# Performance work log

Hardware: AMD Instinct MI355X
Metric: run time of the kernel (lower is better)

The kernel has to match this reference:

```python
import jax, jax.numpy as jnp
import numpy as np

B, S, D_MODEL, H, OUT = 32, 64, 256, 256, 10
N_POS = 64  # n_max_seq + 1


def _coordinate_map():
    i = jnp.arange(N_POS, dtype=jnp.float32)
    r = jnp.sqrt(jnp.float32(N_POS))
    c0 = (i / r - 2.0) / 2.0
    c1 = (jnp.mod(i, r) - 2.0) / 2.0
    coord = jnp.stack([c0, c1], axis=-1)            # [N_POS, 2]
    return jnp.broadcast_to(coord[None], (B, N_POS, 2))


def setup_inputs() -> dict:
    key = jax.random.key(0)
    ks = jax.random.split(key, 13)
    d_in = (D_MODEL + 2) * 3
    w = lambda k, i, o: jax.random.normal(k, (i, o), jnp.float32) * 0.02
    b = lambda k, o: jax.random.normal(k, (o,), jnp.float32) * 0.02
    return {
        'sentences': jax.random.normal(ks[0], (B, S, D_MODEL), jnp.float32),
        'coord': _coordinate_map(),
        'g_w1': w(ks[1], d_in, H), 'g_b1': b(ks[2], H),
        'g_w2': w(ks[3], H, H),    'g_b2': b(ks[4], H),
        'g_w3': w(ks[5], H, H),    'g_b3': b(ks[6], H),
        'f_w1': w(ks[7], H, H),    'f_b1': b(ks[8], H),
        'f_w2': w(ks[9], H, H),    'f_b2': b(ks[10], H),
        'f_w3': w(ks[11], H, OUT), 'f_b3': b(ks[12], OUT),
    }


def reference(sentences, coord, g_w1, g_b1, g_w2, g_b2, g_w3, g_b3,
              f_w1, f_b1, f_w2, f_b2, f_w3, f_b3):
    b, s, d = sentences.shape
    x = jnp.concatenate([sentences, coord[:b, :s, :]], axis=-1)   # [B,S,D+2]
    oi = jnp.broadcast_to(x[:, None, :, :], (b, s, s, d + 2))     # object_i[b,i,j]=x[b,j]
    oj = jnp.broadcast_to(x[:, :, None, :], (b, s, s, d + 2))     # object_j[b,i,j]=x[b,i]
    pairs = jnp.concatenate([oi, oj, oi * oj], axis=-1)           # [B,S,S,3*(D+2)]
    h = jax.nn.relu(jnp.einsum('bijk,kh->bijh', pairs, g_w1) + g_b1)
    h = jax.nn.relu(h @ g_w2 + g_b2)
    h = jax.nn.relu(h @ g_w3 + g_b3)
    rel = h.reshape(b, s * s, -1).sum(axis=1)                     # [B,H]
    y = jax.nn.relu(rel @ f_w1 + f_b1)
    y = jax.nn.relu(y @ f_w2 + f_b2)                              # Dropout: eval mode (identity)
    return y @ f_w3 + f_b3                                        # [B,OUT]
```

## Files before the change

kernel.cpp:

```cpp
#include <hip/hip_runtime.h>
#include <hip/hip_bf16.h>


typedef __attribute__((ext_vector_type(4))) float f32x4;
typedef __attribute__((ext_vector_type(8))) short frag8;

__device__ __forceinline__ float bf2f(short s) {
  return __uint_as_float(((unsigned)(unsigned short)s) << 16);
}
__device__ __forceinline__ short f2bf(float f) {
  unsigned u = __float_as_uint(f);
  return (short)((u + 0x7fffu + ((u >> 16) & 1u)) >> 16);
}

#define KX 288

__global__ __launch_bounds__(256)
void prep(const float* __restrict__ sent, const float* __restrict__ coord,
          const float* __restrict__ g_w1, const float* __restrict__ g_w2,
          const float* __restrict__ g_w3,
          short* __restrict__ xb, short* __restrict__ Wab, short* __restrict__ Wc,
          short* __restrict__ W2t, short* __restrict__ W3t, float* __restrict__ rel) {
  __shared__ short tile[64 * 66];
  const int blk = blockIdx.x, t = threadIdx.x;

  if (blk < 288) {
    long idx0 = ((long)blk * 256 + t) * 8;
#pragma unroll
    for (int e = 0; e < 8; e++) {
      long idx = idx0 + e;
      int row = (int)(idx / KX), k = (int)(idx - (long)row * KX);
      float v = 0.f;
      if (k < 256)      v = sent[(size_t)row * 256 + k];
      else if (k < 258) v = coord[row * 2 + (k - 256)];
      xb[idx] = f2bf(v);
    }
    return;
  }

  const int nc = t & 63, r4 = t >> 6;
  if (blk < 328) {
    int tt = blk - 288, kt = tt >> 3, nt = tt & 7;
    int k0 = kt * 64, n0 = nt * 64;
    for (int p = 0; p < 16; p++) {
      int kl = p * 4 + r4, k = k0 + kl, n = n0 + nc;
      float v = 0.f;
      if (k < 258) {
        int row = (n < 256) ? k : 258 + k;
        int col = (n < 256) ? n : n - 256;
        v = g_w1[(size_t)row * 256 + col];
      }
      tile[kl * 66 + nc] = f2bf(v);
    }
    __syncthreads();
    for (int p = 0; p < 16; p++) {
      int nl = p * 4 + r4;
      if (k0 + nc < KX) Wab[(size_t)(n0 + nl) * KX + k0 + nc] = tile[nc * 66 + nl];
    }
    return;
  }
  if (blk < 348) {
    int tt = blk - 328, kt = tt >> 2, nt = tt & 3;
    int k0 = kt * 64, n0 = nt * 64;
    for (int p = 0; p < 16; p++) {
      int kl = p * 4 + r4, k = k0 + kl;
      float v = (k < 258) ? g_w1[(size_t)(516 + k) * 256 + n0 + nc] : 0.f;
      tile[kl * 66 + nc] = f2bf(v);
    }
    __syncthreads();
    for (int p = 0; p < 16; p++) {
      int nl = p * 4 + r4;
      if (k0 + nc < KX) Wc[(size_t)(n0 + nl) * KX + k0 + nc] = tile[nc * 66 + nl];
    }
    return;
  }
  if (blk < 380) {
    int tt = blk - 348;
    const float* W = (tt < 16) ? g_w2 : g_w3;
    short* Wt = (tt < 16) ? W2t : W3t;
    tt &= 15;
    int k0 = (tt >> 2) * 64, n0 = (tt & 3) * 64;
    for (int p = 0; p < 16; p++) {
      int kl = p * 4 + r4;
      tile[kl * 66 + nc] = f2bf(W[(size_t)(k0 + kl) * 256 + n0 + nc]);
    }
    __syncthreads();
    for (int p = 0; p < 16; p++) {
      int nl = p * 4 + r4;
      Wt[(size_t)(n0 + nl) * 256 + k0 + nc] = tile[nc * 66 + nl];
    }
    return;
  }
  {
    int bb = blk - 380;
    ((f32x4*)rel)[bb * 256 + t] = (f32x4){0.f, 0.f, 0.f, 0.f};
  }
}


__global__ __launch_bounds__(64)
void uv_gemm(const short* __restrict__ xb, const short* __restrict__ Wab,
             const float* __restrict__ g_b1, float* __restrict__ uv) {
  const int m0 = blockIdx.x * 64;
  const int n0 = blockIdx.y * 64;
  const int lane = threadIdx.x;
  const int q = lane >> 4, l16 = lane & 15;

  f32x4 acc[4][4];
#pragma unroll
  for (int mt = 0; mt < 4; mt++)
#pragma unroll
    for (int nt = 0; nt < 4; nt++) acc[mt][nt] = (f32x4){0.f, 0.f, 0.f, 0.f};

  for (int k0 = 0; k0 < KX; k0 += 32) {
    frag8 a[4], bb[4];
#pragma unroll
    for (int mt = 0; mt < 4; mt++)
      a[mt] = *(const frag8*)(xb + (size_t)(m0 + mt * 16 + l16) * KX + k0 + q * 8);
#pragma unroll
    for (int nt = 0; nt < 4; nt++)
      bb[nt] = *(const frag8*)(Wab + (size_t)(n0 + nt * 16 + l16) * KX + k0 + q * 8);
#pragma unroll
    for (int mt = 0; mt < 4; mt++)
#pragma unroll
      for (int nt = 0; nt < 4; nt++)
        acc[mt][nt] = __builtin_amdgcn_mfma_f32_16x16x32_bf16(a[mt], bb[nt], acc[mt][nt], 0, 0, 0);
  }
#pragma unroll
  for (int nt = 0; nt < 4; nt++) {
    int col = n0 + nt * 16 + l16;
    float bias = (col >= 256) ? g_b1[col - 256] : 0.f;
#pragma unroll
    for (int mt = 0; mt < 4; mt++) {
      int m = m0 + mt * 16 + q * 4;
#pragma unroll
      for (int r = 0; r < 4; r++)
        uv[(size_t)(m + r) * 512 + col] = acc[mt][nt][r] + bias;
    }
  }
}


#define AS 296
#define LDS_SHORTS (64 * AS)

__global__ __launch_bounds__(256, 3)
void relnet_main(const short* __restrict__ xb, const short* __restrict__ Wc,
                 const short* __restrict__ W2t, const short* __restrict__ W3t,
                 const float* __restrict__ uv, const float* __restrict__ g_b2,
                 const float* __restrict__ g_b3, float* __restrict__ rel) {
  __shared__ short lds[LDS_SHORTS];

  const int tid = threadIdx.x;
  const int bi = blockIdx.x;
  const int b = bi >> 6, i = bi & 63;
  const int lane = tid & 63, wave = tid >> 6;
  const int q = lane >> 4, l16 = lane & 15;
  const int n0 = wave * 64;
  const int rowbase = b * 64;
  const short* xi = xb + (size_t)(rowbase + i) * KX;

  f32x4 acc[4][4];
#pragma unroll
  for (int mt = 0; mt < 4; mt++)
#pragma unroll
    for (int nt = 0; nt < 4; nt++) acc[mt][nt] = (f32x4){0.f, 0.f, 0.f, 0.f};

#pragma unroll
  for (int it = 0; it < 9; it++) {
    int idx = tid + it * 256;
    int j = idx / 36, k8 = (idx - j * 36) * 8;
    frag8 aj = *(const frag8*)(xb + (size_t)(rowbase + j) * KX + k8);
    frag8 ai = *(const frag8*)(xi + k8);
    frag8 r;
#pragma unroll
    for (int t = 0; t < 8; t++) r[t] = f2bf(bf2f(aj[t]) * bf2f(ai[t]));
    *(frag8*)(&lds[j * AS + k8]) = r;
  }
  __syncthreads();

  {
    frag8 a0[4], b0[4], a1[4], b1[4];
#pragma unroll
    for (int mt = 0; mt < 4; mt++)
      a0[mt] = *(const frag8*)(&lds[(mt * 16 + l16) * AS + q * 8]);
#pragma unroll
    for (int nt = 0; nt < 4; nt++)
      b0[nt] = *(const frag8*)(Wc + (size_t)(n0 + nt * 16 + l16) * KX + q * 8);
#pragma unroll
    for (int ks = 0; ks < 9; ks++) {
      if (ks < 8) {
        int k1 = (ks + 1) * 32;
#pragma unroll
        for (int mt = 0; mt < 4; mt++)
          a1[mt] = *(const frag8*)(&lds[(mt * 16 + l16) * AS + k1 + q * 8]);
#pragma unroll
        for (int nt = 0; nt < 4; nt++)
          b1[nt] = *(const frag8*)(Wc + (size_t)(n0 + nt * 16 + l16) * KX + k1 + q * 8);
      }
#pragma unroll
      for (int mt = 0; mt < 4; mt++)
#pragma unroll
        for (int nt = 0; nt < 4; nt++)
          acc[mt][nt] = __builtin_amdgcn_mfma_f32_16x16x32_bf16(a0[mt], b0[nt], acc[mt][nt], 0, 0, 0);
#pragma unroll
      for (int mt = 0; mt < 4; mt++) a0[mt] = a1[mt];
#pragma unroll
      for (int nt = 0; nt < 4; nt++) b0[nt] = b1[nt];
    }
  }
  __syncthreads();

  {
    const float* ub = uv + (size_t)rowbase * 512;
    const float* vp = uv + (size_t)(rowbase + i) * 512 + 256;
#pragma unroll
    for (int nt = 0; nt < 4; nt++) {
      int col = n0 + nt * 16 + l16;
      float vv = vp[col];
#pragma unroll
      for (int mt = 0; mt < 4; mt++) {
        int jb = mt * 16 + q * 4;
#pragma unroll
        for (int r = 0; r < 4; r++) {
          float val = acc[mt][nt][r] + ub[(size_t)(jb + r) * 512 + col] + vv;
          lds[(jb + r) * AS + col] = f2bf(fmaxf(val, 0.f));
        }
        acc[mt][nt] = (f32x4){0.f, 0.f, 0.f, 0.f};
      }
    }
  }
  __syncthreads();

  {
    frag8 a0[4], b0[4], a1[4], b1[4];
#pragma unroll
    for (int mt = 0; mt < 4; mt++)
      a0[mt] = *(const frag8*)(&lds[(mt * 16 + l16) * AS + q * 8]);
#pragma unroll
    for (int nt = 0; nt < 4; nt++)
      b0[nt] = *(const frag8*)(W2t + (size_t)(n0 + nt * 16 + l16) * 256 + q * 8);
#pragma unroll
    for (int ks = 0; ks < 8; ks++) {
      if (ks < 7) {
        int k1 = (ks + 1) * 32;
#pragma unroll
        for (int mt = 0; mt < 4; mt++)
          a1[mt] = *(const frag8*)(&lds[(mt * 16 + l16) * AS + k1 + q * 8]);
#pragma unroll
        for (int nt = 0; nt < 4; nt++)
          b1[nt] = *(const frag8*)(W2t + (size_t)(n0 + nt * 16 + l16) * 256 + k1 + q * 8);
      }
#pragma unroll
      for (int mt = 0; mt < 4; mt++)
#pragma unroll
        for (int nt = 0; nt < 4; nt++)
          acc[mt][nt] = __builtin_amdgcn_mfma_f32_16x16x32_bf16(a0[mt], b0[nt], acc[mt][nt], 0, 0, 0);
#pragma unroll
      for (int mt = 0; mt < 4; mt++) a0[mt] = a1[mt];
#pragma unroll
      for (int nt = 0; nt < 4; nt++) b0[nt] = b1[nt];
    }
  }
  __syncthreads();
#pragma unroll
  for (int nt = 0; nt < 4; nt++) {
    int col = n0 + nt * 16 + l16;
    float b2 = g_b2[col];
#pragma unroll
    for (int mt = 0; mt < 4; mt++) {
      int jb = mt * 16 + q * 4;
#pragma unroll
      for (int r = 0; r < 4; r++)
        lds[(jb + r) * AS + col] = f2bf(fmaxf(acc[mt][nt][r] + b2, 0.f));
      acc[mt][nt] = (f32x4){0.f, 0.f, 0.f, 0.f};
    }
  }
  __syncthreads();

  {
    frag8 a0[4], b0[4], a1[4], b1[4];
#pragma unroll
    for (int mt = 0; mt < 4; mt++)
      a0[mt] = *(const frag8*)(&lds[(mt * 16 + l16) * AS + q * 8]);
#pragma unroll
    for (int nt = 0; nt < 4; nt++)
      b0[nt] = *(const frag8*)(W3t + (size_t)(n0 + nt * 16 + l16) * 256 + q * 8);
#pragma unroll
    for (int ks = 0; ks < 8; ks++) {
      if (ks < 7) {
        int k1 = (ks + 1) * 32;
#pragma unroll
        for (int mt = 0; mt < 4; mt++)
          a1[mt] = *(const frag8*)(&lds[(mt * 16 + l16) * AS + k1 + q * 8]);
#pragma unroll
        for (int nt = 0; nt < 4; nt++)
          b1[nt] = *(const frag8*)(W3t + (size_t)(n0 + nt * 16 + l16) * 256 + k1 + q * 8);
      }
#pragma unroll
      for (int mt = 0; mt < 4; mt++)
#pragma unroll
        for (int nt = 0; nt < 4; nt++)
          acc[mt][nt] = __builtin_amdgcn_mfma_f32_16x16x32_bf16(a0[mt], b0[nt], acc[mt][nt], 0, 0, 0);
#pragma unroll
      for (int mt = 0; mt < 4; mt++) a0[mt] = a1[mt];
#pragma unroll
      for (int nt = 0; nt < 4; nt++) b0[nt] = b1[nt];
    }
  }
#pragma unroll
  for (int nt = 0; nt < 4; nt++) {
    int col = n0 + nt * 16 + l16;
    float b3 = g_b3[col];
    float s = 0.f;
#pragma unroll
    for (int mt = 0; mt < 4; mt++)
#pragma unroll
      for (int r = 0; r < 4; r++)
        s += fmaxf(acc[mt][nt][r] + b3, 0.f);
    s += __shfl_xor(s, 16, 64);
    s += __shfl_xor(s, 32, 64);
    if (q == 0) atomicAdd(&rel[b * 256 + col], s);
  }
}

__global__ __launch_bounds__(256)
void fnet(const float* __restrict__ rel, const float* __restrict__ f_w1,
          const float* __restrict__ f_b1, const float* __restrict__ f_w2,
          const float* __restrict__ f_b2, const float* __restrict__ f_w3,
          const float* __restrict__ f_b3, float* __restrict__ out) {
  int b = blockIdx.x, t = threadIdx.x;
  __shared__ float y0[256], y1[256], y2[256];
  y0[t] = rel[b * 256 + t];
  __syncthreads();
  float s = f_b1[t];
#pragma unroll 8
  for (int k = 0; k < 256; k++) s += y0[k] * f_w1[k * 256 + t];
  y1[t] = fmaxf(s, 0.f);
  __syncthreads();
  s = f_b2[t];
#pragma unroll 8
  for (int k = 0; k < 256; k++) s += y1[k] * f_w2[k * 256 + t];
  y2[t] = fmaxf(s, 0.f);
  __syncthreads();
  if (t < 10) {
    float s2 = f_b3[t];
#pragma unroll 8
    for (int k = 0; k < 256; k++) s2 += y2[k] * f_w3[k * 10 + t];
    out[b * 10 + t] = s2;
  }
}

extern "C" void kernel_launch(void* const* d_in, const int* in_sizes, int n_in,
                              void* d_out, int out_size, void* d_ws, size_t ws_size,
                              hipStream_t stream) {
  const float* sent  = (const float*)d_in[0];
  const float* coord = (const float*)d_in[1];
  const float* g_w1  = (const float*)d_in[2];
  const float* g_b1  = (const float*)d_in[3];
  const float* g_w2  = (const float*)d_in[4];
  const float* g_b2  = (const float*)d_in[5];
  const float* g_w3  = (const float*)d_in[6];
  const float* g_b3  = (const float*)d_in[7];
  const float* f_w1  = (const float*)d_in[8];
  const float* f_b1  = (const float*)d_in[9];
  const float* f_w2  = (const float*)d_in[10];
  const float* f_b2  = (const float*)d_in[11];
  const float* f_w3  = (const float*)d_in[12];
  const float* f_b3  = (const float*)d_in[13];
  float* out = (float*)d_out;

  char* ws = (char*)d_ws;
  size_t off = 0;
  auto alloc = [&](size_t bytes) {
    char* p = ws + off;
    off += (bytes + 255) & ~(size_t)255;
    return p;
  };
  short* xb  = (short*)alloc((size_t)2048 * KX * 2);
  short* Wab = (short*)alloc((size_t)512 * KX * 2);
  short* Wc  = (short*)alloc((size_t)256 * KX * 2);
  short* W2t = (short*)alloc((size_t)256 * 256 * 2);
  short* W3t = (short*)alloc((size_t)256 * 256 * 2);
  float* uv  = (float*)alloc((size_t)2048 * 512 * 4);
  float* rel = (float*)alloc((size_t)32 * 256 * 4);

  prep<<<388, 256, 0, stream>>>(sent, coord, g_w1, g_w2, g_w3, xb, Wab, Wc, W2t, W3t, rel);
  uv_gemm<<<dim3(32, 8), 64, 0, stream>>>(xb, Wab, g_b1, uv);
  relnet_main<<<2048, 256, 0, stream>>>(xb, Wc, W2t, W3t, uv, g_b2, g_b3, rel);
  fnet<<<32, 256, 0, stream>>>(rel, f_w1, f_b1, f_w2, f_b2, f_w3, f_b3, out);
}
```

Measured before the change: 214.3 us.

## Process two i rows per block with 32x32 MFMA and swizzled LDS

relnet_main now handles two object rows i per block, so each block's M tile grows to 128 and the grid shrinks to 1024 blocks. It switches to the 32x32x16 bf16 MFMA, loads the first-layer K in two halves to fit LDS, and uses an XOR-swizzled 256-wide LDS layout for the hidden activations. The aim is to reuse each weight fragment across twice as many rows and to cut LDS bank conflicts. The costs are a larger accumulator per thread, occupancy reduced to 2 blocks per CU, and an extra barrier for the split K.

```diff
diff --git a/kernel.cpp b/kernel.cpp
--- a/kernel.cpp
+++ b/kernel.cpp
@@ -3,6 +3,7 @@
 
 
 typedef __attribute__((ext_vector_type(4))) float f32x4;
+typedef __attribute__((ext_vector_type(16))) float f32x16;
 typedef __attribute__((ext_vector_type(8))) short frag8;
 
 __device__ __forceinline__ float bf2f(short s) {
@@ -141,10 +142,10 @@
 }
 
 
-#define AS 296
-#define LDS_SHORTS (64 * AS)
-
-__global__ __launch_bounds__(256, 3)
+#define ASH 152
+#define LDS_SHORTS 32768
+
+__global__ __launch_bounds__(256, 2)
 void relnet_main(const short* __restrict__ xb, const short* __restrict__ Wc,
                  const short* __restrict__ W2t, const short* __restrict__ W3t,
                  const float* __restrict__ uv, const float* __restrict__ g_b2,
@@ -153,174 +154,198 @@
 
   const int tid = threadIdx.x;
   const int bi = blockIdx.x;
-  const int b = bi >> 6, i = bi & 63;
+  const int b = bi >> 5, ip = bi & 31;
+  const int i0 = ip * 2;
   const int lane = tid & 63, wave = tid >> 6;
-  const int q = lane >> 4, l16 = lane & 15;
+  const int l32 = lane & 31, half = lane >> 5;
   const int n0 = wave * 64;
   const int rowbase = b * 64;
-  const short* xi = xb + (size_t)(rowbase + i) * KX;
-
-  f32x4 acc[4][4];
+
+  f32x16 acc[4][2];
 #pragma unroll
   for (int mt = 0; mt < 4; mt++)
 #pragma unroll
-    for (int nt = 0; nt < 4; nt++) acc[mt][nt] = (f32x4){0.f, 0.f, 0.f, 0.f};
-
-#pragma unroll
-  for (int it = 0; it < 9; it++) {
-    int idx = tid + it * 256;
-    int j = idx / 36, k8 = (idx - j * 36) * 8;
-    frag8 aj = *(const frag8*)(xb + (size_t)(rowbase + j) * KX + k8);
-    frag8 ai = *(const frag8*)(xi + k8);
-    frag8 r;
-#pragma unroll
-    for (int t = 0; t < 8; t++) r[t] = f2bf(bf2f(aj[t]) * bf2f(ai[t]));
-    *(frag8*)(&lds[j * AS + k8]) = r;
-  }
-  __syncthreads();
-
-  {
-    frag8 a0[4], b0[4], a1[4], b1[4];
-#pragma unroll
-    for (int mt = 0; mt < 4; mt++)
-      a0[mt] = *(const frag8*)(&lds[(mt * 16 + l16) * AS + q * 8]);
-#pragma unroll
-    for (int nt = 0; nt < 4; nt++)
-      b0[nt] = *(const frag8*)(Wc + (size_t)(n0 + nt * 16 + l16) * KX + q * 8);
-#pragma unroll
-    for (int ks = 0; ks < 9; ks++) {
-      if (ks < 8) {
-        int k1 = (ks + 1) * 32;
+    for (int nt = 0; nt < 2; nt++)
+#pragma unroll
+      for (int r = 0; r < 16; r++) acc[mt][nt][r] = 0.f;
+
+#pragma unroll
+  for (int h = 0; h < 2; h++) {
+    const int kbase = h * 144;
+#pragma unroll
+    for (int it = 0; it < 9; it++) {
+      int idx = tid + it * 256;
+      int j = idx / 18, c = idx - j * 18;
+      int k = kbase + c * 8;
+      int jj = j & 63, iL = j >> 6;
+      frag8 aj = *(const frag8*)(xb + (size_t)(rowbase + jj) * KX + k);
+      frag8 ai = *(const frag8*)(xb + (size_t)(rowbase + i0 + iL) * KX + k);
+      frag8 r;
+#pragma unroll
+      for (int t = 0; t < 8; t++) r[t] = f2bf(bf2f(aj[t]) * bf2f(ai[t]));
+      *(frag8*)(&lds[j * ASH + c * 8]) = r;
+    }
+    __syncthreads();
+
+    {
+      frag8 a0[4], b0[2], a1[4], b1[2];
+#pragma unroll
+      for (int mt = 0; mt < 4; mt++)
+        a0[mt] = *(const frag8*)(&lds[(mt * 32 + l32) * ASH + half * 8]);
+#pragma unroll
+      for (int nt = 0; nt < 2; nt++)
+        b0[nt] = *(const frag8*)(Wc + (size_t)(n0 + nt * 32 + l32) * KX + kbase + half * 8);
+#pragma unroll
+      for (int ks = 0; ks < 9; ks++) {
+        if (ks < 8) {
+          int k1 = (ks + 1) * 16 + half * 8;
+#pragma unroll
+          for (int mt = 0; mt < 4; mt++)
+            a1[mt] = *(const frag8*)(&lds[(mt * 32 + l32) * ASH + k1]);
+#pragma unroll
+          for (int nt = 0; nt < 2; nt++)
+            b1[nt] = *(const frag8*)(Wc + (size_t)(n0 + nt * 32 + l32) * KX + kbase + k1);
+        }
 #pragma unroll
         for (int mt = 0; mt < 4; mt++)
-          a1[mt] = *(const frag8*)(&lds[(mt * 16 + l16) * AS + k1 + q * 8]);
-#pragma unroll
-        for (int nt = 0; nt < 4; nt++)
-          b1[nt] = *(const frag8*)(Wc + (size_t)(n0 + nt * 16 + l16) * KX + k1 + q * 8);
-      }
-#pragma unroll
-      for (int mt = 0; mt < 4; mt++)
-#pragma unroll
-        for (int nt = 0; nt < 4; nt++)
-          acc[mt][nt] = __builtin_amdgcn_mfma_f32_16x16x32_bf16(a0[mt], b0[nt], acc[mt][nt], 0, 0, 0);
-#pragma unroll
-      for (int mt = 0; mt < 4; mt++) a0[mt] = a1[mt];
-#pragma unroll
-      for (int nt = 0; nt < 4; nt++) b0[nt] = b1[nt];
-    }
-  }
-  __syncthreads();
+#pragma unroll
+          for (int nt = 0; nt < 2; nt++)
+            acc[mt][nt] = __builtin_amdgcn_mfma_f32_32x32x16_bf16(a0[mt], b0[nt], acc[mt][nt], 0, 0, 0);
+#pragma unroll
+        for (int mt = 0; mt < 4; mt++) a0[mt] = a1[mt];
+#pragma unroll
+        for (int nt = 0; nt < 2; nt++) b0[nt] = b1[nt];
+      }
+    }
+    __syncthreads();
+  }
 
   {
     const float* ub = uv + (size_t)rowbase * 512;
-    const float* vp = uv + (size_t)(rowbase + i) * 512 + 256;
-#pragma unroll
-    for (int nt = 0; nt < 4; nt++) {
-      int col = n0 + nt * 16 + l16;
-      float vv = vp[col];
+    const float* v0p = uv + (size_t)(rowbase + i0) * 512 + 256;
+    const float* v1p = uv + (size_t)(rowbase + i0 + 1) * 512 + 256;
+#pragma unroll
+    for (int nt = 0; nt < 2; nt++) {
+      int col = n0 + nt * 32 + l32;
+      int cb = (n0 + nt * 32) >> 3;
+      float vv0 = v0p[col], vv1 = v1p[col];
 #pragma unroll
       for (int mt = 0; mt < 4; mt++) {
-        int jb = mt * 16 + q * 4;
-#pragma unroll
-        for (int r = 0; r < 4; r++) {
-          float val = acc[mt][nt][r] + ub[(size_t)(jb + r) * 512 + col] + vv;
-          lds[(jb + r) * AS + col] = f2bf(fmaxf(val, 0.f));
+        float vv = (mt < 2) ? vv0 : vv1;
+#pragma unroll
+        for (int r = 0; r < 16; r++) {
+          int rowbits = (r & 3) + 8 * (r >> 2) + 4 * half;
+          int jm = (mt & 1) * 32 + rowbits;
+          int m = mt * 32 + rowbits;
+          float val = acc[mt][nt][r] + ub[(size_t)jm * 512 + col] + vv;
+          int sw = (r & 3) + 4 * half;
+          lds[m * 256 + (((cb + (l32 >> 3)) ^ sw) << 3) + (l32 & 7)] = f2bf(fmaxf(val, 0.f));
         }
-        acc[mt][nt] = (f32x4){0.f, 0.f, 0.f, 0.f};
+#pragma unroll
+        for (int r = 0; r < 16; r++) acc[mt][nt][r] = 0.f;
       }
     }
   }
   __syncthreads();
 
   {
-    frag8 a0[4], b0[4], a1[4], b1[4];
+    const int swr = l32 & 7;
+    frag8 a0[4], b0[2], a1[4], b1[2];
 #pragma unroll
     for (int mt = 0; mt < 4; mt++)
-      a0[mt] = *(const frag8*)(&lds[(mt * 16 + l16) * AS + q * 8]);
-#pragma unroll
-    for (int nt = 0; nt < 4; nt++)
-      b0[nt] = *(const frag8*)(W2t + (size_t)(n0 + nt * 16 + l16) * 256 + q * 8);
-#pragma unroll
-    for (int ks = 0; ks < 8; ks++) {
-      if (ks < 7) {
-        int k1 = (ks + 1) * 32;
+      a0[mt] = *(const frag8*)(&lds[(mt * 32 + l32) * 256 + ((half ^ swr) << 3)]);
+#pragma unroll
+    for (int nt = 0; nt < 2; nt++)
+      b0[nt] = *(const frag8*)(W2t + (size_t)(n0 + nt * 32 + l32) * 256 + half * 8);
+#pragma unroll
+    for (int ks = 0; ks < 16; ks++) {
+      if (ks < 15) {
+        int c1 = ((2 * (ks + 1) + half) ^ swr) << 3;
+        int k1 = (ks + 1) * 16 + half * 8;
 #pragma unroll
         for (int mt = 0; mt < 4; mt++)
-          a1[mt] = *(const frag8*)(&lds[(mt * 16 + l16) * AS + k1 + q * 8]);
-#pragma unroll
-        for (int nt = 0; nt < 4; nt++)
-          b1[nt] = *(const frag8*)(W2t + (size_t)(n0 + nt * 16 + l16) * 256 + k1 + q * 8);
+          a1[mt] = *(const frag8*)(&lds[(mt * 32 + l32) * 256 + c1]);
+#pragma unroll
+        for (int nt = 0; nt < 2; nt++)
+          b1[nt] = *(const frag8*)(W2t + (size_t)(n0 + nt * 32 + l32) * 256 + k1);
       }
 #pragma unroll
       for (int mt = 0; mt < 4; mt++)
 #pragma unroll
-        for (int nt = 0; nt < 4; nt++)
-          acc[mt][nt] = __builtin_amdgcn_mfma_f32_16x16x32_bf16(a0[mt], b0[nt], acc[mt][nt], 0, 0, 0);
+        for (int nt = 0; nt < 2; nt++)
+          acc[mt][nt] = __builtin_amdgcn_mfma_f32_32x32x16_bf16(a0[mt], b0[nt], acc[mt][nt], 0, 0, 0);
 #pragma unroll
       for (int mt = 0; mt < 4; mt++) a0[mt] = a1[mt];
 #pragma unroll
-      for (int nt = 0; nt < 4; nt++) b0[nt] = b1[nt];
-    }
-  }
-  __syncthreads();
-#pragma unroll
-  for (int nt = 0; nt < 4; nt++) {
-    int col = n0 + nt * 16 + l16;
+      for (int nt = 0; nt < 2; nt++) b0[nt] = b1[nt];
+    }
+  }
+  __syncthreads();
+#pragma unroll
+  for (int nt = 0; nt < 2; nt++) {
+    int col = n0 + nt * 32 + l32;
+    int cb = (n0 + nt * 32) >> 3;
     float b2 = g_b2[col];
 #pragma unroll
     for (int mt = 0; mt < 4; mt++) {
-      int jb = mt * 16 + q * 4;
-#pragma unroll
-      for (int r = 0; r < 4; r++)
-        lds[(jb + r) * AS + col] = f2bf(fmaxf(acc[mt][nt][r] + b2, 0.f));
-      acc[mt][nt] = (f32x4){0.f, 0.f, 0.f, 0.f};
+#pragma unroll
+      for (int r = 0; r < 16; r++) {
+        int rowbits = (r & 3) + 8 * (r >> 2) + 4 * half;
+        int m = mt * 32 + rowbits;
+        int sw = (r & 3) + 4 * half;
+        lds[m * 256 + (((cb + (l32 >> 3)) ^ sw) << 3) + (l32 & 7)] =
+            f2bf(fmaxf(acc[mt][nt][r] + b2, 0.f));
+      }
+#pragma unroll
+      for (int r = 0; r < 16; r++) acc[mt][nt][r] = 0.f;
     }
   }
   __syncthreads();
 
   {
-    frag8 a0[4], b0[4], a1[4], b1[4];
+    const int swr = l32 & 7;
+    frag8 a0[4], b0[2], a1[4], b1[2];
 #pragma unroll
     for (int mt = 0; mt < 4; mt++)
-      a0[mt] = *(const frag8*)(&lds[(mt * 16 + l16) * AS + q * 8]);
-#pragma unroll
-    for (int nt = 0; nt < 4; nt++)
-      b0[nt] = *(const frag8*)(W3t + (size_t)(n0 + nt * 16 + l16) * 256 + q * 8);
-#pragma unroll
-    for (int ks = 0; ks < 8; ks++) {
-      if (ks < 7) {
-        int k1 = (ks + 1) * 32;
+      a0[mt] = *(const frag8*)(&lds[(mt * 32 + l32) * 256 + ((half ^ swr) << 3)]);
+#pragma unroll
+    for (int nt = 0; nt < 2; nt++)
+      b0[nt] = *(const frag8*)(W3t + (size_t)(n0 + nt * 32 + l32) * 256 + half * 8);
+#pragma unroll
+    for (int ks = 0; ks < 16; ks++) {
+      if (ks < 15) {
+        int c1 = ((2 * (ks + 1) + half) ^ swr) << 3;
+        int k1 = (ks + 1) * 16 + half * 8;
 #pragma unroll
         for (int mt = 0; mt < 4; mt++)
-          a1[mt] = *(const frag8*)(&lds[(mt * 16 + l16) * AS + k1 + q * 8]);
-#pragma unroll
-        for (int nt = 0; nt < 4; nt++)
-          b1[nt] = *(const frag8*)(W3t + (size_t)(n0 + nt * 16 + l16) * 256 + k1 + q * 8);
+          a1[mt] = *(const frag8*)(&lds[(mt * 32 + l32) * 256 + c1]);
+#pragma unroll
+        for (int nt = 0; nt < 2; nt++)
+          b1[nt] = *(const frag8*)(W3t + (size_t)(n0 + nt * 32 + l32) * 256 + k1);
       }
 #pragma unroll
       for (int mt = 0; mt < 4; mt++)
 #pragma unroll
-        for (int nt = 0; nt < 4; nt++)
-          acc[mt][nt] = __builtin_amdgcn_mfma_f32_16x16x32_bf16(a0[mt], b0[nt], acc[mt][nt], 0, 0, 0);
+        for (int nt = 0; nt < 2; nt++)
+          acc[mt][nt] = __builtin_amdgcn_mfma_f32_32x32x16_bf16(a0[mt], b0[nt], acc[mt][nt], 0, 0, 0);
 #pragma unroll
       for (int mt = 0; mt < 4; mt++) a0[mt] = a1[mt];
 #pragma unroll
-      for (int nt = 0; nt < 4; nt++) b0[nt] = b1[nt];
-    }
-  }
-#pragma unroll
-  for (int nt = 0; nt < 4; nt++) {
-    int col = n0 + nt * 16 + l16;
+      for (int nt = 0; nt < 2; nt++) b0[nt] = b1[nt];
+    }
+  }
+#pragma unroll
+  for (int nt = 0; nt < 2; nt++) {
+    int col = n0 + nt * 32 + l32;
     float b3 = g_b3[col];
     float s = 0.f;
 #pragma unroll
     for (int mt = 0; mt < 4; mt++)
 #pragma unroll
-      for (int r = 0; r < 4; r++)
+      for (int r = 0; r < 16; r++)
         s += fmaxf(acc[mt][nt][r] + b3, 0.f);
-    s += __shfl_xor(s, 16, 64);
     s += __shfl_xor(s, 32, 64);
-    if (q == 0) atomicAdd(&rel[b * 256 + col], s);
+    if (half == 0) atomicAdd(&rel[b * 256 + col], s);
   }
 }
 
@@ -387,6 +412,6 @@
 
   prep<<<388, 256, 0, stream>>>(sent, coord, g_w1, g_w2, g_w3, xb, Wab, Wc, W2t, W3t, rel);
   uv_gemm<<<dim3(32, 8), 64, 0, stream>>>(xb, Wab, g_b1, uv);
-  relnet_main<<<2048, 256, 0, stream>>>(xb, Wc, W2t, W3t, uv, g_b2, g_b3, rel);
+  relnet_main<<<1024, 256, 0, stream>>>(xb, Wc, W2t, W3t, uv, g_b2, g_b3, rel);
   fnet<<<32, 256, 0, stream>>>(rel, f_w1, f_b1, f_w2, f_b2, f_w3, f_b3, out);
 }
```

After: 184.6 us. -13.9%, faster.
